# Kernel tuning notes

Measured on AMD Instinct MI355X. Metric: run time of the kernel, lower is better.

Reference implementation:

```python
import jax, jax.numpy as jnp
import numpy as np

OBS_DIM, GOAL_DIM, NUM_SKILLS, ACTION_DIM = 256, 64, 16, 32
HIDDEN = 128
BATCH = 65536


def setup_inputs() -> dict:
    key = jax.random.key(0)
    ks = jax.random.split(key, 10)
    s = lambda k, shape, fan_in: jax.random.normal(k, shape, jnp.float32) * (1.0 / np.sqrt(fan_in))
    return {
        "obs": jax.random.normal(ks[0], (BATCH, OBS_DIM), jnp.float32),
        "goals": jax.random.normal(ks[1], (BATCH, GOAL_DIM), jnp.float32),
        # gate (AlphaNet) params
        "Wa1": s(ks[2], (OBS_DIM + GOAL_DIM, HIDDEN), OBS_DIM + GOAL_DIM),
        "ba1": jnp.zeros((HIDDEN,), jnp.float32),
        "Wa2": s(ks[3], (HIDDEN, NUM_SKILLS), HIDDEN),
        "ba2": jnp.zeros((NUM_SKILLS,), jnp.float32),
        # stacked executor params: [S, in, out]
        "W1": s(ks[4], (NUM_SKILLS, OBS_DIM, HIDDEN), OBS_DIM),
        "b1": jnp.zeros((NUM_SKILLS, HIDDEN), jnp.float32),
        "W2": s(ks[5], (NUM_SKILLS, HIDDEN, ACTION_DIM), HIDDEN),
        "b2": jnp.zeros((NUM_SKILLS, ACTION_DIM), jnp.float32),
    }


def reference(obs, goals, Wa1, ba1, Wa2, ba2, W1, b1, W2, b2):
    # gate: softmax(Linear(ReLU(Linear(cat(obs, goals)))))
    concat_input = jnp.concatenate([obs, goals], axis=-1)  # [B, O+G]
    ha = jax.nn.relu(concat_input @ Wa1 + ba1)             # [B, H]
    alphas = jax.nn.softmax(ha @ Wa2 + ba2, axis=-1)       # [B, S]

    # all experts as one grouped GEMM over stacked weights
    h = jax.nn.relu(jnp.einsum("bo,soh->bsh", obs, W1) + b1[None])  # [B, S, H]
    skill_outputs = jnp.einsum("bsh,sha->bsa", h, W2) + b2[None]    # [B, S, A]

    # weighted sum over skills
    mixed_action = jnp.einsum("bsa,bs->ba", skill_outputs, alphas)  # [B, A]
    return mixed_action, alphas
```

## Files before the change

### kernel.cpp

```cpp
#include <hip/hip_runtime.h>


typedef __attribute__((ext_vector_type(8))) short    bf16x8;
typedef __attribute__((ext_vector_type(4))) float    f32x4;
typedef __attribute__((ext_vector_type(4))) _Float16 f16x4;
using half2v = decltype(__builtin_amdgcn_cvt_pkrtz(0.f, 0.f));

#define GATE_W1_OFF   0
#define GATE_W2_OFF   81920
#define GATE_BA1_OFF  86016
#define GATE_BA2_OFF  86528
#define GATE_BYTES    86592
#define S_W1_STRIDE   528
#define S_W2_OFF      67584
#define S_W2_STRIDE   272
#define S_B1_OFF      76288
#define S_B2_OFF      76800
#define S_IMG         76928
#define LDS_BYTES     163520

__device__ __forceinline__ unsigned short f2bf(float f) {
  unsigned u = __builtin_bit_cast(unsigned, f);
  return (unsigned short)((u + 0x7FFFu + ((u >> 16) & 1u)) >> 16);
}

__device__ __forceinline__ bf16x8 pack_bf8(f32x4 a, f32x4 b) {
  int4 r;
  asm("v_cvt_pk_bf16_f32 %0, %1, %2" : "=v"(r.x) : "v"(a[0]), "v"(a[1]));
  asm("v_cvt_pk_bf16_f32 %0, %1, %2" : "=v"(r.y) : "v"(a[2]), "v"(a[3]));
  asm("v_cvt_pk_bf16_f32 %0, %1, %2" : "=v"(r.z) : "v"(b[0]), "v"(b[1]));
  asm("v_cvt_pk_bf16_f32 %0, %1, %2" : "=v"(r.w) : "v"(b[2]), "v"(b[3]));
  return __builtin_bit_cast(bf16x8, r);
}

#define RELU_SCALE_PACK(dst, v, av, z)                                   \
  {                                                                      \
    half2v lo_ = __builtin_amdgcn_cvt_pkrtz((v)[0], (v)[1]);             \
    half2v hi_ = __builtin_amdgcn_cvt_pkrtz((v)[2], (v)[3]);             \
    lo_ = __builtin_elementwise_max(lo_, z) * (av);                      \
    hi_ = __builtin_elementwise_max(hi_, z) * (av);                      \
    dst[0] = (_Float16)lo_[0]; dst[1] = (_Float16)lo_[1];                \
    dst[2] = (_Float16)hi_[0]; dst[3] = (_Float16)hi_[1];                \
  }

__global__ void prep_weights(const float* __restrict__ Wa1, const float* __restrict__ Wa2,
                             const float* __restrict__ ba1, const float* __restrict__ ba2,
                             const float* __restrict__ W1,  const float* __restrict__ W2,
                             const float* __restrict__ b1,  const float* __restrict__ b2,
                             unsigned char* __restrict__ ws) {
  int i = blockIdx.x * 256 + threadIdx.x;
  if (i < 524288) {
    int s = i >> 15, r = i & 32767, h = r >> 8, o = r & 255;
    float v = W1[(s * 256 + o) * 128 + h];
    *(unsigned short*)(ws + GATE_BYTES + s * S_IMG + h * S_W1_STRIDE + 2 * o) = f2bf(v);
  } else if (i < 589824) {
    int j = i - 524288, s = j >> 12, r = j & 4095, a = r >> 7, h = r & 127;
    float v = W2[(s * 128 + h) * 32 + a];
    *(_Float16*)(ws + GATE_BYTES + s * S_IMG + S_W2_OFF + a * S_W2_STRIDE + 2 * h) =
        (_Float16)v;
  } else if (i < 630784) {
    int j = i - 589824, h = j / 320, o = j - h * 320;
    float v = Wa1[o * 128 + h];
    *(unsigned short*)(ws + GATE_W1_OFF + h * 640 +
                       ((2 * o) ^ ((h & 7) << 4))) = f2bf(v);
  } else if (i < 632832) {
    int j = i - 630784, n = j >> 7, h = j & 127;
    float v = Wa2[h * 16 + n];
    *(_Float16*)(ws + GATE_W2_OFF + n * 256 +
                 ((2 * h) ^ ((n & 7) << 3))) = (_Float16)v;
  } else if (i < 634880) {
    int j = i - 632832, s = j >> 7, h = j & 127;
    *(float*)(ws + GATE_BYTES + s * S_IMG + S_B1_OFF + 4 * h) = b1[s * 128 + h];
  } else if (i < 635392) {
    int j = i - 634880, s = j >> 5, a = j & 31;
    *(float*)(ws + GATE_BYTES + s * S_IMG + S_B2_OFF + 4 * a) = b2[s * 32 + a];
  } else if (i < 635520) {
    int j = i - 635392;
    *(float*)(ws + GATE_BA1_OFF + 4 * j) = ba1[j];
  } else if (i < 635536) {
    int j = i - 635520;
    *(float*)(ws + GATE_BA2_OFF + 4 * j) = ba2[j];
  }
}

__device__ __forceinline__ void stage_lin(const unsigned char* gsrc, unsigned char* ldst,
                                          int tid, int bytes) {
  for (int off = tid * 16; off < bytes; off += 512 * 16) {
    __builtin_amdgcn_global_load_lds(
        (const __attribute__((address_space(1))) unsigned int*)(const void*)(gsrc + off),
        (__attribute__((address_space(3))) unsigned int*)(void*)(ldst + off), 16, 0, 0);
  }
}

__global__ __launch_bounds__(512, 2)
void mop_fused(const float* __restrict__ obs, const float* __restrict__ goals,
               const unsigned char* __restrict__ ws, float* __restrict__ dout) {
  extern __shared__ unsigned char smem[];
  const int tid  = threadIdx.x;
  const int lane = tid & 63;
  const int wave = tid >> 6;
  const int l15  = lane & 15;
  const int g    = lane >> 4;
  const int swz4 = (lane & 7) << 4;
  const int swz3 = (lane & 7) << 3;
  const int rowbase = blockIdx.x * 256 + wave * 32;

  float* out_mixed = dout;
  float* out_alpha = dout + 65536 * 32;

  const int lw1 = l15 * S_W1_STRIDE + 16 * g;
  const int lw2 = S_W2_OFF + l15 * S_W2_STRIDE + 8 * g;
  const int lb  = 16 * g;

  stage_lin(ws, smem, tid, GATE_BYTES);

  bf16x8 obsf[2][8];
  bf16x8 goalf[2][2];
  #pragma unroll
  for (int nb = 0; nb < 2; ++nb) {
    const float* rp = obs + (size_t)(rowbase + nb * 16 + l15) * 256 + 8 * g;
    #pragma unroll
    for (int t = 0; t < 8; ++t) {
      f32x4 a = *(const f32x4*)(rp + 32 * t);
      f32x4 c = *(const f32x4*)(rp + 32 * t + 4);
      obsf[nb][t] = pack_bf8(a, c);
    }
    const float* gp = goals + (size_t)(rowbase + nb * 16 + l15) * 64 + 8 * g;
    #pragma unroll
    for (int t = 0; t < 2; ++t) {
      f32x4 a = *(const f32x4*)(gp + 32 * t);
      f32x4 c = *(const f32x4*)(gp + 32 * t + 4);
      goalf[nb][t] = pack_bf8(a, c);
    }
  }

  __syncthreads();

  stage_lin(ws + GATE_BYTES, smem + GATE_BYTES, tid, S_IMG);

  f32x4 gacc[2][8];
  #pragma unroll
  for (int ht = 0; ht < 8; ++ht) {
    f32x4 bias = *(const f32x4*)(smem + GATE_BA1_OFF + 64 * ht + lb);
    gacc[0][ht] = bias; gacc[1][ht] = bias;
  }
  #pragma unroll
  for (int t = 0; t < 10; ++t) {
    bf16x8 bf0 = (t < 8) ? obsf[0][t] : goalf[0][t - 8];
    bf16x8 bf1 = (t < 8) ? obsf[1][t] : goalf[1][t - 8];
    #pragma unroll
    for (int ht = 0; ht < 8; ++ht) {
      int row = 16 * ht + l15;
      bf16x8 af = *(const bf16x8*)(smem + GATE_W1_OFF + row * 640 +
                                   ((64 * t + 16 * g) ^ swz4));
      gacc[0][ht] = __builtin_amdgcn_mfma_f32_16x16x32_bf16(af, bf0, gacc[0][ht], 0, 0, 0);
      gacc[1][ht] = __builtin_amdgcn_mfma_f32_16x16x32_bf16(af, bf1, gacc[1][ht], 0, 0, 0);
    }
  }

  const half2v zh = __builtin_amdgcn_cvt_pkrtz(0.f, 0.f);
  f32x4 alph[2];
  #pragma unroll
  for (int nb = 0; nb < 2; ++nb) {
    f32x4 lacc = *(const f32x4*)(smem + GATE_BA2_OFF + lb);
    #pragma unroll
    for (int ht = 0; ht < 8; ++ht) {
      f32x4 v = gacc[nb][ht];
      f16x4 hf;
      {
        half2v lo_ = __builtin_amdgcn_cvt_pkrtz(v[0], v[1]);
        half2v hi_ = __builtin_amdgcn_cvt_pkrtz(v[2], v[3]);
        lo_ = __builtin_elementwise_max(lo_, zh);
        hi_ = __builtin_elementwise_max(hi_, zh);
        hf[0] = (_Float16)lo_[0]; hf[1] = (_Float16)lo_[1];
        hf[2] = (_Float16)hi_[0]; hf[3] = (_Float16)hi_[1];
      }
      f16x4 wf = *(const f16x4*)(smem + GATE_W2_OFF + l15 * 256 +
                                 ((32 * ht + 8 * g) ^ swz3));
      lacc = __builtin_amdgcn_mfma_f32_16x16x16f16(wf, hf, lacc, 0, 0, 0);
    }
    float m = fmaxf(fmaxf(lacc[0], lacc[1]), fmaxf(lacc[2], lacc[3]));
    m = fmaxf(m, __shfl_xor(m, 16, 64));
    m = fmaxf(m, __shfl_xor(m, 32, 64));
    f32x4 e;
    e[0] = __expf(lacc[0] - m); e[1] = __expf(lacc[1] - m);
    e[2] = __expf(lacc[2] - m); e[3] = __expf(lacc[3] - m);
    float ssum = e[0] + e[1] + e[2] + e[3];
    ssum += __shfl_xor(ssum, 16, 64);
    ssum += __shfl_xor(ssum, 32, 64);
    float inv = 1.0f / ssum;
    alph[nb] = e * inv;
    *(f32x4*)(out_alpha + (size_t)(rowbase + nb * 16 + l15) * 16 + 4 * g) = alph[nb];
  }

  __syncthreads();

  f32x4 macc[2][2] = {};
  for (int s = 0; s < 16; ++s) {
    const unsigned char* buf = smem + ((s & 1) ? 0 : GATE_BYTES);
    if (s < 15) {
      unsigned char* nbuf = smem + (((s + 1) & 1) ? 0 : GATE_BYTES);
      stage_lin(ws + GATE_BYTES + (size_t)(s + 1) * S_IMG, nbuf, tid, S_IMG);
    }
    f32x4 acc[2][8];
    #pragma unroll
    for (int ht = 0; ht < 8; ++ht) {
      f32x4 b1v = *(const f32x4*)(buf + S_B1_OFF + 64 * ht + lb);
      acc[0][ht] = b1v; acc[1][ht] = b1v;
    }

    const int asrc = ((s >> 2) << 4) | l15;
    float p0 = (s & 1) ? alph[0][1] : alph[0][0];
    float p1 = (s & 1) ? alph[0][3] : alph[0][2];
    float as0 = __shfl((s & 2) ? p1 : p0, asrc, 64);
    float q0 = (s & 1) ? alph[1][1] : alph[1][0];
    float q1 = (s & 1) ? alph[1][3] : alph[1][2];
    float as1 = __shfl((s & 2) ? q1 : q0, asrc, 64);
    const half2v a0h = __builtin_amdgcn_cvt_pkrtz(as0, as0);
    const half2v a1h = __builtin_amdgcn_cvt_pkrtz(as1, as1);

    const unsigned char* w1p = buf + lw1;
    const unsigned char* w2p = buf + lw2;

    __builtin_amdgcn_s_setprio(1);
    #pragma unroll
    for (int t = 0; t < 8; ++t) {
      const unsigned char* w1t = w1p + t * 64;
      #pragma unroll
      for (int ht = 0; ht < 8; ++ht) {
        bf16x8 af = *(const bf16x8*)(w1t + ht * 8448);
        acc[0][ht] = __builtin_amdgcn_mfma_f32_16x16x32_bf16(af, obsf[0][t], acc[0][ht], 0, 0, 0);
        acc[1][ht] = __builtin_amdgcn_mfma_f32_16x16x32_bf16(af, obsf[1][t], acc[1][ht], 0, 0, 0);
      }
    }
    #pragma unroll
    for (int ht = 0; ht < 8; ++ht) {
      f16x4 hf0, hf1;
      RELU_SCALE_PACK(hf0, acc[0][ht], a0h, zh);
      RELU_SCALE_PACK(hf1, acc[1][ht], a1h, zh);
      #pragma unroll
      for (int ta = 0; ta < 2; ++ta) {
        f16x4 wf = *(const f16x4*)(w2p + ta * 4352 + ht * 32);
        macc[0][ta] = __builtin_amdgcn_mfma_f32_16x16x16f16(wf, hf0, macc[0][ta], 0, 0, 0);
        macc[1][ta] = __builtin_amdgcn_mfma_f32_16x16x16f16(wf, hf1, macc[1][ta], 0, 0, 0);
      }
    }
    __builtin_amdgcn_s_setprio(0);
    #pragma unroll
    for (int ta = 0; ta < 2; ++ta) {
      f32x4 b2v = *(const f32x4*)(buf + S_B2_OFF + 64 * ta + lb);
      macc[0][ta] = macc[0][ta] + b2v * as0;
      macc[1][ta] = macc[1][ta] + b2v * as1;
    }
    __syncthreads();
  }

  #pragma unroll
  for (int nb = 0; nb < 2; ++nb) {
    #pragma unroll
    for (int ta = 0; ta < 2; ++ta) {
      *(f32x4*)(out_mixed + (size_t)(rowbase + nb * 16 + l15) * 32 + 16 * ta + 4 * g) =
          macc[nb][ta];
    }
  }
}

extern "C" void kernel_launch(void* const* d_in, const int* in_sizes, int n_in,
                              void* d_out, int out_size, void* d_ws, size_t ws_size,
                              hipStream_t stream) {
  const float* obs   = (const float*)d_in[0];
  const float* goals = (const float*)d_in[1];
  const float* Wa1   = (const float*)d_in[2];
  const float* ba1   = (const float*)d_in[3];
  const float* Wa2   = (const float*)d_in[4];
  const float* ba2   = (const float*)d_in[5];
  const float* W1    = (const float*)d_in[6];
  const float* b1    = (const float*)d_in[7];
  const float* W2    = (const float*)d_in[8];
  const float* b2    = (const float*)d_in[9];
  unsigned char* ws  = (unsigned char*)d_ws;
  float* out = (float*)d_out;

  prep_weights<<<2483, 256, 0, stream>>>(Wa1, Wa2, ba1, ba2, W1, W2, b1, b2, ws);
  mop_fused<<<256, 512, LDS_BYTES, stream>>>(obs, goals, ws, out);
}
```

Measured before the change: 93.70 us.

## Software-pipeline skill loop across halves and hoist biases into a single LDS block

Splits each skill's hidden dimension into two halves and defers the second half's ReLU/scale and second GEMM into the next iteration. This interleaves the W1 MFMA chain with W2 MFMAs and places the next-skill weight staging between the two halves. Biases for all skills are staged once into a separate LDS region, with b2 stored as bf16, which shrinks the per-skill image. The aim is to hide the dependency and latency of the second-layer GEMMs and the staging. The cost is an extra barrier per iteration, more live registers, and bf16 rounding of b2.

```diff
diff --git a/kernel.cpp b/kernel.cpp
--- a/kernel.cpp
+++ b/kernel.cpp
@@ -4,6 +4,7 @@
 typedef __attribute__((ext_vector_type(8))) short    bf16x8;
 typedef __attribute__((ext_vector_type(4))) float    f32x4;
 typedef __attribute__((ext_vector_type(4))) _Float16 f16x4;
+typedef __attribute__((ext_vector_type(4))) short    s16x4;
 using half2v = decltype(__builtin_amdgcn_cvt_pkrtz(0.f, 0.f));
 
 #define GATE_W1_OFF   0
@@ -14,14 +15,21 @@
 #define S_W1_STRIDE   528
 #define S_W2_OFF      67584
 #define S_W2_STRIDE   272
-#define S_B1_OFF      76288
-#define S_B2_OFF      76800
-#define S_IMG         76928
-#define LDS_BYTES     163520
+#define S_IMG         76288
+#define BIAS_LDS      76928
+#define B2_LDS        85120
+#define BIAS_BYTES    9216
+#define LDS_BYTES     162880
+#define BIAS_WS       1307200
 
 __device__ __forceinline__ unsigned short f2bf(float f) {
   unsigned u = __builtin_bit_cast(unsigned, f);
   return (unsigned short)((u + 0x7FFFu + ((u >> 16) & 1u)) >> 16);
+}
+
+__device__ __forceinline__ float bf2f(short s) {
+  unsigned u = ((unsigned)(unsigned short)s) << 16;
+  return __builtin_bit_cast(float, u);
 }
 
 __device__ __forceinline__ bf16x8 pack_bf8(f32x4 a, f32x4 b) {
@@ -69,11 +77,11 @@
     *(_Float16*)(ws + GATE_W2_OFF + n * 256 +
                  ((2 * h) ^ ((n & 7) << 3))) = (_Float16)v;
   } else if (i < 634880) {
-    int j = i - 632832, s = j >> 7, h = j & 127;
-    *(float*)(ws + GATE_BYTES + s * S_IMG + S_B1_OFF + 4 * h) = b1[s * 128 + h];
+    int j = i - 632832;
+    *(float*)(ws + BIAS_WS + 4 * j) = b1[j];
   } else if (i < 635392) {
-    int j = i - 634880, s = j >> 5, a = j & 31;
-    *(float*)(ws + GATE_BYTES + s * S_IMG + S_B2_OFF + 4 * a) = b2[s * 32 + a];
+    int j = i - 634880;
+    *(unsigned short*)(ws + BIAS_WS + 8192 + 2 * j) = f2bf(b2[j]);
   } else if (i < 635520) {
     int j = i - 635392;
     *(float*)(ws + GATE_BA1_OFF + 4 * j) = ba1[j];
@@ -195,20 +203,26 @@
 
   __syncthreads();
 
+  stage_lin(ws + BIAS_WS, smem + BIAS_LDS, tid, BIAS_BYTES);
+
+  f32x4 accA[2][4], accB[2][4];
   f32x4 macc[2][2] = {};
+  half2v a0hP = zh, a1hP = zh;
+  float as0P = 0.f, as1P = 0.f;
+  const unsigned char* w2pP = smem;
+
   for (int s = 0; s < 16; ++s) {
     const unsigned char* buf = smem + ((s & 1) ? 0 : GATE_BYTES);
-    if (s < 15) {
-      unsigned char* nbuf = smem + (((s + 1) & 1) ? 0 : GATE_BYTES);
-      stage_lin(ws + GATE_BYTES + (size_t)(s + 1) * S_IMG, nbuf, tid, S_IMG);
-    }
-    f32x4 acc[2][8];
-    #pragma unroll
-    for (int ht = 0; ht < 8; ++ht) {
-      f32x4 b1v = *(const f32x4*)(buf + S_B1_OFF + 64 * ht + lb);
-      acc[0][ht] = b1v; acc[1][ht] = b1v;
-    }
-
+    const unsigned char* w1p = buf + lw1;
+    const unsigned char* w2p = buf + lw2;
+
+    __syncthreads();
+
+    __builtin_amdgcn_s_setprio(1);
+    f32x4 b1v[8];
+    #pragma unroll
+    for (int ht = 0; ht < 8; ++ht)
+      b1v[ht] = *(const f32x4*)(smem + BIAS_LDS + s * 512 + 64 * ht + lb);
     const int asrc = ((s >> 2) << 4) | l15;
     float p0 = (s & 1) ? alph[0][1] : alph[0][0];
     float p1 = (s & 1) ? alph[0][3] : alph[0][2];
@@ -219,40 +233,100 @@
     const half2v a0h = __builtin_amdgcn_cvt_pkrtz(as0, as0);
     const half2v a1h = __builtin_amdgcn_cvt_pkrtz(as1, as1);
 
-    const unsigned char* w1p = buf + lw1;
-    const unsigned char* w2p = buf + lw2;
-
-    __builtin_amdgcn_s_setprio(1);
+    #pragma unroll
+    for (int hl = 0; hl < 4; ++hl) { accA[0][hl] = b1v[hl]; accA[1][hl] = b1v[hl]; }
     #pragma unroll
     for (int t = 0; t < 8; ++t) {
       const unsigned char* w1t = w1p + t * 64;
       #pragma unroll
-      for (int ht = 0; ht < 8; ++ht) {
-        bf16x8 af = *(const bf16x8*)(w1t + ht * 8448);
-        acc[0][ht] = __builtin_amdgcn_mfma_f32_16x16x32_bf16(af, obsf[0][t], acc[0][ht], 0, 0, 0);
-        acc[1][ht] = __builtin_amdgcn_mfma_f32_16x16x32_bf16(af, obsf[1][t], acc[1][ht], 0, 0, 0);
-      }
-    }
-    #pragma unroll
-    for (int ht = 0; ht < 8; ++ht) {
+      for (int hl = 0; hl < 4; ++hl) {
+        bf16x8 af = *(const bf16x8*)(w1t + hl * 8448);
+        accA[0][hl] = __builtin_amdgcn_mfma_f32_16x16x32_bf16(af, obsf[0][t], accA[0][hl], 0, 0, 0);
+        accA[1][hl] = __builtin_amdgcn_mfma_f32_16x16x32_bf16(af, obsf[1][t], accA[1][hl], 0, 0, 0);
+      }
+    }
+    if (s > 0) {
+      #pragma unroll
+      for (int hl = 0; hl < 4; ++hl) {
+        f16x4 hf0, hf1;
+        RELU_SCALE_PACK(hf0, accB[0][hl], a0hP, zh);
+        RELU_SCALE_PACK(hf1, accB[1][hl], a1hP, zh);
+        #pragma unroll
+        for (int ta = 0; ta < 2; ++ta) {
+          f16x4 wf = *(const f16x4*)(w2pP + ta * 4352 + (4 + hl) * 32);
+          macc[0][ta] = __builtin_amdgcn_mfma_f32_16x16x16f16(wf, hf0, macc[0][ta], 0, 0, 0);
+          macc[1][ta] = __builtin_amdgcn_mfma_f32_16x16x16f16(wf, hf1, macc[1][ta], 0, 0, 0);
+        }
+      }
+      #pragma unroll
+      for (int ta = 0; ta < 2; ++ta) {
+        s16x4 raw = *(const s16x4*)(smem + B2_LDS + (s - 1) * 64 + (16 * ta + 4 * g) * 2);
+        f32x4 b2v;
+        b2v[0] = bf2f(raw[0]); b2v[1] = bf2f(raw[1]);
+        b2v[2] = bf2f(raw[2]); b2v[3] = bf2f(raw[3]);
+        macc[0][ta] = macc[0][ta] + b2v * as0P;
+        macc[1][ta] = macc[1][ta] + b2v * as1P;
+      }
+    }
+    __builtin_amdgcn_s_setprio(0);
+
+    __syncthreads();
+
+    if (s < 15) {
+      unsigned char* nbuf = smem + (((s + 1) & 1) ? 0 : GATE_BYTES);
+      stage_lin(ws + GATE_BYTES + (size_t)(s + 1) * S_IMG, nbuf, tid, S_IMG);
+    }
+
+    __builtin_amdgcn_s_setprio(1);
+    #pragma unroll
+    for (int hl = 0; hl < 4; ++hl) { accB[0][hl] = b1v[4 + hl]; accB[1][hl] = b1v[4 + hl]; }
+    #pragma unroll
+    for (int t = 0; t < 8; ++t) {
+      const unsigned char* w1t = w1p + t * 64;
+      #pragma unroll
+      for (int hl = 0; hl < 4; ++hl) {
+        bf16x8 af = *(const bf16x8*)(w1t + (4 + hl) * 8448);
+        accB[0][hl] = __builtin_amdgcn_mfma_f32_16x16x32_bf16(af, obsf[0][t], accB[0][hl], 0, 0, 0);
+        accB[1][hl] = __builtin_amdgcn_mfma_f32_16x16x32_bf16(af, obsf[1][t], accB[1][hl], 0, 0, 0);
+      }
+    }
+    #pragma unroll
+    for (int hl = 0; hl < 4; ++hl) {
       f16x4 hf0, hf1;
-      RELU_SCALE_PACK(hf0, acc[0][ht], a0h, zh);
-      RELU_SCALE_PACK(hf1, acc[1][ht], a1h, zh);
+      RELU_SCALE_PACK(hf0, accA[0][hl], a0h, zh);
+      RELU_SCALE_PACK(hf1, accA[1][hl], a1h, zh);
       #pragma unroll
       for (int ta = 0; ta < 2; ++ta) {
-        f16x4 wf = *(const f16x4*)(w2p + ta * 4352 + ht * 32);
+        f16x4 wf = *(const f16x4*)(w2p + ta * 4352 + hl * 32);
         macc[0][ta] = __builtin_amdgcn_mfma_f32_16x16x16f16(wf, hf0, macc[0][ta], 0, 0, 0);
         macc[1][ta] = __builtin_amdgcn_mfma_f32_16x16x16f16(wf, hf1, macc[1][ta], 0, 0, 0);
       }
     }
     __builtin_amdgcn_s_setprio(0);
+
+    a0hP = a0h; a1hP = a1h; as0P = as0; as1P = as1; w2pP = w2p;
+  }
+
+  #pragma unroll
+  for (int hl = 0; hl < 4; ++hl) {
+    f16x4 hf0, hf1;
+    RELU_SCALE_PACK(hf0, accB[0][hl], a0hP, zh);
+    RELU_SCALE_PACK(hf1, accB[1][hl], a1hP, zh);
     #pragma unroll
     for (int ta = 0; ta < 2; ++ta) {
-      f32x4 b2v = *(const f32x4*)(buf + S_B2_OFF + 64 * ta + lb);
-      macc[0][ta] = macc[0][ta] + b2v * as0;
-      macc[1][ta] = macc[1][ta] + b2v * as1;
-    }
-    __syncthreads();
+      f16x4 wf = *(const f16x4*)(w2pP + ta * 4352 + (4 + hl) * 32);
+      macc[0][ta] = __builtin_amdgcn_mfma_f32_16x16x16f16(wf, hf0, macc[0][ta], 0, 0, 0);
+      macc[1][ta] = __builtin_amdgcn_mfma_f32_16x16x16f16(wf, hf1, macc[1][ta], 0, 0, 0);
+    }
+  }
+  #pragma unroll
+  for (int ta = 0; ta < 2; ++ta) {
+    s16x4 raw = *(const s16x4*)(smem + B2_LDS + 15 * 64 + (16 * ta + 4 * g) * 2);
+    f32x4 b2v;
+    b2v[0] = bf2f(raw[0]); b2v[1] = bf2f(raw[1]);
+    b2v[2] = bf2f(raw[2]); b2v[3] = bf2f(raw[3]);
+    macc[0][ta] = macc[0][ta] + b2v * as0P;
+    macc[1][ta] = macc[1][ta] + b2v * as1P;
   }
 
   #pragma unroll
```

Measured after the change: 94.62 us. Within noise of the previous version (+1.0%).

## Switch executor GEMMs to 32x32x16 MFMA with permuted weight layout

Applied to the files above, without the earlier changes.

The per-skill executor matmuls move from 16x16x32 and 16x16x16 MFMA tiles to 32x32x16 bf16/f16 MFMA. The prep kernel permutes W1 rows, b1 and b2 so the 32x32 accumulator layout feeds the second GEMM directly. Obs is reloaded from global in a 32-row fragment layout. The mixed output is transposed through an LDS scratch area so each store is a contiguous row. The aim is fewer MFMA issues and fewer weight LDS reads per FLOP, at the cost of a second global read of obs and extra LDS traffic in the epilogue.

```diff
diff --git a/kernel.cpp b/kernel.cpp
--- a/kernel.cpp
+++ b/kernel.cpp
@@ -1,9 +1,11 @@
 #include <hip/hip_runtime.h>
 
 
-typedef __attribute__((ext_vector_type(8))) short    bf16x8;
-typedef __attribute__((ext_vector_type(4))) float    f32x4;
-typedef __attribute__((ext_vector_type(4))) _Float16 f16x4;
+typedef __attribute__((ext_vector_type(8)))  short    bf16x8;
+typedef __attribute__((ext_vector_type(4)))  float    f32x4;
+typedef __attribute__((ext_vector_type(16))) float    f32x16;
+typedef __attribute__((ext_vector_type(4)))  _Float16 f16x4;
+typedef __attribute__((ext_vector_type(8)))  _Float16 f16x8;
 using half2v = decltype(__builtin_amdgcn_cvt_pkrtz(0.f, 0.f));
 
 #define GATE_W1_OFF   0
@@ -33,16 +35,6 @@
   return __builtin_bit_cast(bf16x8, r);
 }
 
-#define RELU_SCALE_PACK(dst, v, av, z)                                   \
-  {                                                                      \
-    half2v lo_ = __builtin_amdgcn_cvt_pkrtz((v)[0], (v)[1]);             \
-    half2v hi_ = __builtin_amdgcn_cvt_pkrtz((v)[2], (v)[3]);             \
-    lo_ = __builtin_elementwise_max(lo_, z) * (av);                      \
-    hi_ = __builtin_elementwise_max(hi_, z) * (av);                      \
-    dst[0] = (_Float16)lo_[0]; dst[1] = (_Float16)lo_[1];                \
-    dst[2] = (_Float16)hi_[0]; dst[3] = (_Float16)hi_[1];                \
-  }
-
 __global__ void prep_weights(const float* __restrict__ Wa1, const float* __restrict__ Wa2,
                              const float* __restrict__ ba1, const float* __restrict__ ba2,
                              const float* __restrict__ W1,  const float* __restrict__ W2,
@@ -51,8 +43,9 @@
   int i = blockIdx.x * 256 + threadIdx.x;
   if (i < 524288) {
     int s = i >> 15, r = i & 32767, h = r >> 8, o = r & 255;
+    int hp = (h & ~12) | ((h & 4) << 1) | ((h & 8) >> 1);
     float v = W1[(s * 256 + o) * 128 + h];
-    *(unsigned short*)(ws + GATE_BYTES + s * S_IMG + h * S_W1_STRIDE + 2 * o) = f2bf(v);
+    *(unsigned short*)(ws + GATE_BYTES + s * S_IMG + hp * S_W1_STRIDE + 2 * o) = f2bf(v);
   } else if (i < 589824) {
     int j = i - 524288, s = j >> 12, r = j & 4095, a = r >> 7, h = r & 127;
     float v = W2[(s * 128 + h) * 32 + a];
@@ -70,10 +63,12 @@
                  ((2 * h) ^ ((n & 7) << 3))) = (_Float16)v;
   } else if (i < 634880) {
     int j = i - 632832, s = j >> 7, h = j & 127;
-    *(float*)(ws + GATE_BYTES + s * S_IMG + S_B1_OFF + 4 * h) = b1[s * 128 + h];
+    int hp = (h & ~12) | ((h & 4) << 1) | ((h & 8) >> 1);
+    *(float*)(ws + GATE_BYTES + s * S_IMG + S_B1_OFF + 4 * hp) = b1[s * 128 + h];
   } else if (i < 635392) {
-    int j = i - 634880, s = j >> 5, a = j & 31;
-    *(float*)(ws + GATE_BYTES + s * S_IMG + S_B2_OFF + 4 * a) = b2[s * 32 + a];
+    int j = i - 634880, s = j >> 5, p = j & 31;
+    int a = (p & 3) | ((p & 4) << 1) | ((p & 8) << 1) | ((p & 16) >> 2);
+    *(float*)(ws + GATE_BYTES + s * S_IMG + S_B2_OFF + 4 * p) = b2[s * 32 + a];
   } else if (i < 635520) {
     int j = i - 635392;
     *(float*)(ws + GATE_BA1_OFF + 4 * j) = ba1[j];
@@ -101,6 +96,8 @@
   const int wave = tid >> 6;
   const int l15  = lane & 15;
   const int g    = lane >> 4;
+  const int r31  = lane & 31;
+  const int hi   = lane >> 5;
   const int swz4 = (lane & 7) << 4;
   const int swz3 = (lane & 7) << 3;
   const int rowbase = blockIdx.x * 256 + wave * 32;
@@ -108,107 +105,110 @@
   float* out_mixed = dout;
   float* out_alpha = dout + 65536 * 32;
 
-  const int lw1 = l15 * S_W1_STRIDE + 16 * g;
-  const int lw2 = S_W2_OFF + l15 * S_W2_STRIDE + 8 * g;
-  const int lb  = 16 * g;
-
   stage_lin(ws, smem, tid, GATE_BYTES);
-
-  bf16x8 obsf[2][8];
-  bf16x8 goalf[2][2];
-  #pragma unroll
-  for (int nb = 0; nb < 2; ++nb) {
-    const float* rp = obs + (size_t)(rowbase + nb * 16 + l15) * 256 + 8 * g;
-    #pragma unroll
-    for (int t = 0; t < 8; ++t) {
-      f32x4 a = *(const f32x4*)(rp + 32 * t);
-      f32x4 c = *(const f32x4*)(rp + 32 * t + 4);
-      obsf[nb][t] = pack_bf8(a, c);
-    }
-    const float* gp = goals + (size_t)(rowbase + nb * 16 + l15) * 64 + 8 * g;
-    #pragma unroll
-    for (int t = 0; t < 2; ++t) {
-      f32x4 a = *(const f32x4*)(gp + 32 * t);
-      f32x4 c = *(const f32x4*)(gp + 32 * t + 4);
-      goalf[nb][t] = pack_bf8(a, c);
-    }
-  }
-
-  __syncthreads();
-
-  stage_lin(ws + GATE_BYTES, smem + GATE_BYTES, tid, S_IMG);
-
-  f32x4 gacc[2][8];
-  #pragma unroll
-  for (int ht = 0; ht < 8; ++ht) {
-    f32x4 bias = *(const f32x4*)(smem + GATE_BA1_OFF + 64 * ht + lb);
-    gacc[0][ht] = bias; gacc[1][ht] = bias;
-  }
-  #pragma unroll
-  for (int t = 0; t < 10; ++t) {
-    bf16x8 bf0 = (t < 8) ? obsf[0][t] : goalf[0][t - 8];
-    bf16x8 bf1 = (t < 8) ? obsf[1][t] : goalf[1][t - 8];
-    #pragma unroll
-    for (int ht = 0; ht < 8; ++ht) {
-      int row = 16 * ht + l15;
-      bf16x8 af = *(const bf16x8*)(smem + GATE_W1_OFF + row * 640 +
-                                   ((64 * t + 16 * g) ^ swz4));
-      gacc[0][ht] = __builtin_amdgcn_mfma_f32_16x16x32_bf16(af, bf0, gacc[0][ht], 0, 0, 0);
-      gacc[1][ht] = __builtin_amdgcn_mfma_f32_16x16x32_bf16(af, bf1, gacc[1][ht], 0, 0, 0);
-    }
-  }
 
   const half2v zh = __builtin_amdgcn_cvt_pkrtz(0.f, 0.f);
   f32x4 alph[2];
-  #pragma unroll
-  for (int nb = 0; nb < 2; ++nb) {
-    f32x4 lacc = *(const f32x4*)(smem + GATE_BA2_OFF + lb);
+  {
+    bf16x8 gobs[2][8];
+    bf16x8 goalf[2][2];
+    #pragma unroll
+    for (int nb = 0; nb < 2; ++nb) {
+      const float* rp = obs + (size_t)(rowbase + nb * 16 + l15) * 256 + 8 * g;
+      #pragma unroll
+      for (int t = 0; t < 8; ++t) {
+        f32x4 a = *(const f32x4*)(rp + 32 * t);
+        f32x4 c = *(const f32x4*)(rp + 32 * t + 4);
+        gobs[nb][t] = pack_bf8(a, c);
+      }
+      const float* gp = goals + (size_t)(rowbase + nb * 16 + l15) * 64 + 8 * g;
+      #pragma unroll
+      for (int t = 0; t < 2; ++t) {
+        f32x4 a = *(const f32x4*)(gp + 32 * t);
+        f32x4 c = *(const f32x4*)(gp + 32 * t + 4);
+        goalf[nb][t] = pack_bf8(a, c);
+      }
+    }
+
+    __syncthreads();
+    stage_lin(ws + GATE_BYTES, smem + GATE_BYTES, tid, S_IMG);
+
+    f32x4 gacc[2][8];
     #pragma unroll
     for (int ht = 0; ht < 8; ++ht) {
-      f32x4 v = gacc[nb][ht];
-      f16x4 hf;
-      {
-        half2v lo_ = __builtin_amdgcn_cvt_pkrtz(v[0], v[1]);
-        half2v hi_ = __builtin_amdgcn_cvt_pkrtz(v[2], v[3]);
-        lo_ = __builtin_elementwise_max(lo_, zh);
-        hi_ = __builtin_elementwise_max(hi_, zh);
-        hf[0] = (_Float16)lo_[0]; hf[1] = (_Float16)lo_[1];
-        hf[2] = (_Float16)hi_[0]; hf[3] = (_Float16)hi_[1];
-      }
-      f16x4 wf = *(const f16x4*)(smem + GATE_W2_OFF + l15 * 256 +
-                                 ((32 * ht + 8 * g) ^ swz3));
-      lacc = __builtin_amdgcn_mfma_f32_16x16x16f16(wf, hf, lacc, 0, 0, 0);
-    }
-    float m = fmaxf(fmaxf(lacc[0], lacc[1]), fmaxf(lacc[2], lacc[3]));
-    m = fmaxf(m, __shfl_xor(m, 16, 64));
-    m = fmaxf(m, __shfl_xor(m, 32, 64));
-    f32x4 e;
-    e[0] = __expf(lacc[0] - m); e[1] = __expf(lacc[1] - m);
-    e[2] = __expf(lacc[2] - m); e[3] = __expf(lacc[3] - m);
-    float ssum = e[0] + e[1] + e[2] + e[3];
-    ssum += __shfl_xor(ssum, 16, 64);
-    ssum += __shfl_xor(ssum, 32, 64);
-    float inv = 1.0f / ssum;
-    alph[nb] = e * inv;
-    *(f32x4*)(out_alpha + (size_t)(rowbase + nb * 16 + l15) * 16 + 4 * g) = alph[nb];
+      f32x4 bias = *(const f32x4*)(smem + GATE_BA1_OFF + 64 * ht + 16 * g);
+      gacc[0][ht] = bias; gacc[1][ht] = bias;
+    }
+    #pragma unroll
+    for (int t = 0; t < 10; ++t) {
+      bf16x8 bf0 = (t < 8) ? gobs[0][t] : goalf[0][t - 8];
+      bf16x8 bf1 = (t < 8) ? gobs[1][t] : goalf[1][t - 8];
+      #pragma unroll
+      for (int ht = 0; ht < 8; ++ht) {
+        int row = 16 * ht + l15;
+        bf16x8 af = *(const bf16x8*)(smem + GATE_W1_OFF + row * 640 +
+                                     ((64 * t + 16 * g) ^ swz4));
+        gacc[0][ht] = __builtin_amdgcn_mfma_f32_16x16x32_bf16(af, bf0, gacc[0][ht], 0, 0, 0);
+        gacc[1][ht] = __builtin_amdgcn_mfma_f32_16x16x32_bf16(af, bf1, gacc[1][ht], 0, 0, 0);
+      }
+    }
+    #pragma unroll
+    for (int nb = 0; nb < 2; ++nb) {
+      f32x4 lacc = *(const f32x4*)(smem + GATE_BA2_OFF + 16 * g);
+      #pragma unroll
+      for (int ht = 0; ht < 8; ++ht) {
+        f32x4 v = gacc[nb][ht];
+        f16x4 hf;
+        {
+          half2v lo_ = __builtin_amdgcn_cvt_pkrtz(v[0], v[1]);
+          half2v hi_ = __builtin_amdgcn_cvt_pkrtz(v[2], v[3]);
+          lo_ = __builtin_elementwise_max(lo_, zh);
+          hi_ = __builtin_elementwise_max(hi_, zh);
+          hf[0] = (_Float16)lo_[0]; hf[1] = (_Float16)lo_[1];
+          hf[2] = (_Float16)hi_[0]; hf[3] = (_Float16)hi_[1];
+        }
+        f16x4 wf = *(const f16x4*)(smem + GATE_W2_OFF + l15 * 256 +
+                                   ((32 * ht + 8 * g) ^ swz3));
+        lacc = __builtin_amdgcn_mfma_f32_16x16x16f16(wf, hf, lacc, 0, 0, 0);
+      }
+      float m = fmaxf(fmaxf(lacc[0], lacc[1]), fmaxf(lacc[2], lacc[3]));
+      m = fmaxf(m, __shfl_xor(m, 16, 64));
+      m = fmaxf(m, __shfl_xor(m, 32, 64));
+      f32x4 e;
+      e[0] = __expf(lacc[0] - m); e[1] = __expf(lacc[1] - m);
+      e[2] = __expf(lacc[2] - m); e[3] = __expf(lacc[3] - m);
+      float ssum = e[0] + e[1] + e[2] + e[3];
+      ssum += __shfl_xor(ssum, 16, 64);
+      ssum += __shfl_xor(ssum, 32, 64);
+      float inv = 1.0f / ssum;
+      alph[nb] = e * inv;
+      *(f32x4*)(out_alpha + (size_t)(rowbase + nb * 16 + l15) * 16 + 4 * g) = alph[nb];
+    }
+  }
+
+  bf16x8 obsf[16];
+  {
+    const float* rp2 = obs + (size_t)(rowbase + r31) * 256 + 8 * hi;
+    #pragma unroll
+    for (int t = 0; t < 16; ++t) {
+      f32x4 a = *(const f32x4*)(rp2 + 16 * t);
+      f32x4 c = *(const f32x4*)(rp2 + 16 * t + 4);
+      obsf[t] = pack_bf8(a, c);
+    }
   }
 
   __syncthreads();
 
-  f32x4 macc[2][2] = {};
+  const int lw1 = r31 * S_W1_STRIDE + 16 * hi;
+  const int lw2 = S_W2_OFF + r31 * S_W2_STRIDE + 16 * hi;
+
+  f32x16 macc = {};
   for (int s = 0; s < 16; ++s) {
     const unsigned char* buf = smem + ((s & 1) ? 0 : GATE_BYTES);
     if (s < 15) {
       unsigned char* nbuf = smem + (((s + 1) & 1) ? 0 : GATE_BYTES);
       stage_lin(ws + GATE_BYTES + (size_t)(s + 1) * S_IMG, nbuf, tid, S_IMG);
     }
-    f32x4 acc[2][8];
-    #pragma unroll
-    for (int ht = 0; ht < 8; ++ht) {
-      f32x4 b1v = *(const f32x4*)(buf + S_B1_OFF + 64 * ht + lb);
-      acc[0][ht] = b1v; acc[1][ht] = b1v;
-    }
-
     const int asrc = ((s >> 2) << 4) | l15;
     float p0 = (s & 1) ? alph[0][1] : alph[0][0];
     float p1 = (s & 1) ? alph[0][3] : alph[0][2];
@@ -216,52 +216,84 @@
     float q0 = (s & 1) ? alph[1][1] : alph[1][0];
     float q1 = (s & 1) ? alph[1][3] : alph[1][2];
     float as1 = __shfl((s & 2) ? q1 : q0, asrc, 64);
-    const half2v a0h = __builtin_amdgcn_cvt_pkrtz(as0, as0);
-    const half2v a1h = __builtin_amdgcn_cvt_pkrtz(as1, as1);
+    const float av = (r31 >> 4) ? as1 : as0;
+    const half2v avh = __builtin_amdgcn_cvt_pkrtz(av, av);
 
     const unsigned char* w1p = buf + lw1;
     const unsigned char* w2p = buf + lw2;
 
+    f32x16 acc[4];
+    #pragma unroll
+    for (int ht = 0; ht < 4; ++ht) {
+      f32x4 c0 = *(const f32x4*)(buf + S_B1_OFF + (32 * ht + 4 * hi) * 4);
+      f32x4 c1 = *(const f32x4*)(buf + S_B1_OFF + (32 * ht + 8 + 4 * hi) * 4);
+      f32x4 c2 = *(const f32x4*)(buf + S_B1_OFF + (32 * ht + 16 + 4 * hi) * 4);
+      f32x4 c3 = *(const f32x4*)(buf + S_B1_OFF + (32 * ht + 24 + 4 * hi) * 4);
+      acc[ht][0]  = c0[0]; acc[ht][1]  = c0[1]; acc[ht][2]  = c0[2]; acc[ht][3]  = c0[3];
+      acc[ht][4]  = c1[0]; acc[ht][5]  = c1[1]; acc[ht][6]  = c1[2]; acc[ht][7]  = c1[3];
+      acc[ht][8]  = c2[0]; acc[ht][9]  = c2[1]; acc[ht][10] = c2[2]; acc[ht][11] = c2[3];
+      acc[ht][12] = c3[0]; acc[ht][13] = c3[1]; acc[ht][14] = c3[2]; acc[ht][15] = c3[3];
+    }
+
     __builtin_amdgcn_s_setprio(1);
     #pragma unroll
-    for (int t = 0; t < 8; ++t) {
-      const unsigned char* w1t = w1p + t * 64;
-      #pragma unroll
-      for (int ht = 0; ht < 8; ++ht) {
-        bf16x8 af = *(const bf16x8*)(w1t + ht * 8448);
-        acc[0][ht] = __builtin_amdgcn_mfma_f32_16x16x32_bf16(af, obsf[0][t], acc[0][ht], 0, 0, 0);
-        acc[1][ht] = __builtin_amdgcn_mfma_f32_16x16x32_bf16(af, obsf[1][t], acc[1][ht], 0, 0, 0);
-      }
-    }
-    #pragma unroll
-    for (int ht = 0; ht < 8; ++ht) {
-      f16x4 hf0, hf1;
-      RELU_SCALE_PACK(hf0, acc[0][ht], a0h, zh);
-      RELU_SCALE_PACK(hf1, acc[1][ht], a1h, zh);
-      #pragma unroll
-      for (int ta = 0; ta < 2; ++ta) {
-        f16x4 wf = *(const f16x4*)(w2p + ta * 4352 + ht * 32);
-        macc[0][ta] = __builtin_amdgcn_mfma_f32_16x16x16f16(wf, hf0, macc[0][ta], 0, 0, 0);
-        macc[1][ta] = __builtin_amdgcn_mfma_f32_16x16x16f16(wf, hf1, macc[1][ta], 0, 0, 0);
+    for (int t = 0; t < 16; ++t) {
+      const unsigned char* w1t = w1p + t * 32;
+      #pragma unroll
+      for (int ht = 0; ht < 4; ++ht) {
+        bf16x8 af = *(const bf16x8*)(w1t + ht * 16896);
+        acc[ht] = __builtin_amdgcn_mfma_f32_32x32x16_bf16(af, obsf[t], acc[ht], 0, 0, 0);
+      }
+    }
+    #pragma unroll
+    for (int ht = 0; ht < 4; ++ht) {
+      #pragma unroll
+      for (int q = 0; q < 2; ++q) {
+        const int t2 = 2 * ht + q;
+        int4 w;
+        {
+          half2v h0 = __builtin_amdgcn_cvt_pkrtz(acc[ht][8 * q + 0], acc[ht][8 * q + 1]);
+          half2v h1 = __builtin_amdgcn_cvt_pkrtz(acc[ht][8 * q + 2], acc[ht][8 * q + 3]);
+          half2v h2 = __builtin_amdgcn_cvt_pkrtz(acc[ht][8 * q + 4], acc[ht][8 * q + 5]);
+          half2v h3 = __builtin_amdgcn_cvt_pkrtz(acc[ht][8 * q + 6], acc[ht][8 * q + 7]);
+          h0 = __builtin_elementwise_max(h0, zh) * avh;
+          h1 = __builtin_elementwise_max(h1, zh) * avh;
+          h2 = __builtin_elementwise_max(h2, zh) * avh;
+          h3 = __builtin_elementwise_max(h3, zh) * avh;
+          w.x = __builtin_bit_cast(int, h0); w.y = __builtin_bit_cast(int, h1);
+          w.z = __builtin_bit_cast(int, h2); w.w = __builtin_bit_cast(int, h3);
+        }
+        f16x8 hf = __builtin_bit_cast(f16x8, w);
+        f16x8 w2f = *(const f16x8*)(w2p + t2 * 32);
+        macc = __builtin_amdgcn_mfma_f32_32x32x16_f16(w2f, hf, macc, 0, 0, 0);
       }
     }
     __builtin_amdgcn_s_setprio(0);
-    #pragma unroll
-    for (int ta = 0; ta < 2; ++ta) {
-      f32x4 b2v = *(const f32x4*)(buf + S_B2_OFF + 64 * ta + lb);
-      macc[0][ta] = macc[0][ta] + b2v * as0;
-      macc[1][ta] = macc[1][ta] + b2v * as1;
+    {
+      f32x4 d0 = *(const f32x4*)(buf + S_B2_OFF + (16 * hi + 0) * 4);
+      f32x4 d1 = *(const f32x4*)(buf + S_B2_OFF + (16 * hi + 4) * 4);
+      f32x4 d2 = *(const f32x4*)(buf + S_B2_OFF + (16 * hi + 8) * 4);
+      f32x4 d3 = *(const f32x4*)(buf + S_B2_OFF + (16 * hi + 12) * 4);
+      macc[0]  += av * d0[0]; macc[1]  += av * d0[1]; macc[2]  += av * d0[2]; macc[3]  += av * d0[3];
+      macc[4]  += av * d1[0]; macc[5]  += av * d1[1]; macc[6]  += av * d1[2]; macc[7]  += av * d1[3];
+      macc[8]  += av * d2[0]; macc[9]  += av * d2[1]; macc[10] += av * d2[2]; macc[11] += av * d2[3];
+      macc[12] += av * d3[0]; macc[13] += av * d3[1]; macc[14] += av * d3[2]; macc[15] += av * d3[3];
     }
     __syncthreads();
   }
 
+  unsigned char* scr = smem + wave * 4352;
   #pragma unroll
-  for (int nb = 0; nb < 2; ++nb) {
-    #pragma unroll
-    for (int ta = 0; ta < 2; ++ta) {
-      *(f32x4*)(out_mixed + (size_t)(rowbase + nb * 16 + l15) * 32 + 16 * ta + 4 * g) =
-          macc[nb][ta];
-    }
+  for (int r = 0; r < 16; ++r) {
+    const int a = (r & 3) | ((r & 4) << 1) | ((r & 8) << 1) | (hi << 2);
+    *(float*)(scr + (r31 * 33 + a) * 4) = macc[r];
+  }
+  __syncthreads();
+  const int r2 = lane >> 1, c16 = (lane & 1) * 16;
+  #pragma unroll
+  for (int k = 0; k < 4; ++k) {
+    f32x4 v = *(const f32x4*)(scr + (r2 * 33 + c16 + 4 * k) * 4);
+    *(f32x4*)(out_mixed + (size_t)(rowbase + r2) * 32 + c16 + 4 * k) = v;
   }
 }
 
```

After: 103.3 us. 10.3% more time.

## Split fused kernel into separate gate and skill-expert kernels

Applied to the files above, without the earlier changes.

The single fused kernel is split into a gate kernel that writes alphas to the output buffer and a skill kernel that reads them back from global memory. The skill kernel uses 256-thread blocks with a single-buffered LDS image of about 77KB, so two blocks can share a CU instead of one large block. The weight staging is no longer double-buffered: each expert's weights are loaded after the previous compute finishes, behind two barriers, so load latency is exposed. It also adds an extra kernel launch, reloads obs in both kernels, and does scalar global reads of alpha on every skill iteration.

```diff
diff --git a/kernel.cpp b/kernel.cpp
--- a/kernel.cpp
+++ b/kernel.cpp
@@ -17,7 +17,6 @@
 #define S_B1_OFF      76288
 #define S_B2_OFF      76800
 #define S_IMG         76928
-#define LDS_BYTES     163520
 
 __device__ __forceinline__ unsigned short f2bf(float f) {
   unsigned u = __builtin_bit_cast(unsigned, f);
@@ -83,18 +82,19 @@
   }
 }
 
+template <int NT>
 __device__ __forceinline__ void stage_lin(const unsigned char* gsrc, unsigned char* ldst,
                                           int tid, int bytes) {
-  for (int off = tid * 16; off < bytes; off += 512 * 16) {
+  for (int off = tid * 16; off < bytes; off += NT * 16) {
     __builtin_amdgcn_global_load_lds(
         (const __attribute__((address_space(1))) unsigned int*)(const void*)(gsrc + off),
         (__attribute__((address_space(3))) unsigned int*)(void*)(ldst + off), 16, 0, 0);
   }
 }
 
-__global__ __launch_bounds__(512, 2)
-void mop_fused(const float* __restrict__ obs, const float* __restrict__ goals,
-               const unsigned char* __restrict__ ws, float* __restrict__ dout) {
+__global__ __launch_bounds__(512, 1)
+void mop_gate(const float* __restrict__ obs, const float* __restrict__ goals,
+              const unsigned char* __restrict__ ws, float* __restrict__ dout) {
   extern __shared__ unsigned char smem[];
   const int tid  = threadIdx.x;
   const int lane = tid & 63;
@@ -105,14 +105,9 @@
   const int swz3 = (lane & 7) << 3;
   const int rowbase = blockIdx.x * 256 + wave * 32;
 
-  float* out_mixed = dout;
   float* out_alpha = dout + 65536 * 32;
 
-  const int lw1 = l15 * S_W1_STRIDE + 16 * g;
-  const int lw2 = S_W2_OFF + l15 * S_W2_STRIDE + 8 * g;
-  const int lb  = 16 * g;
-
-  stage_lin(ws, smem, tid, GATE_BYTES);
+  stage_lin<512>(ws, smem, tid, GATE_BYTES);
 
   bf16x8 obsf[2][8];
   bf16x8 goalf[2][2];
@@ -136,12 +131,10 @@
 
   __syncthreads();
 
-  stage_lin(ws + GATE_BYTES, smem + GATE_BYTES, tid, S_IMG);
-
   f32x4 gacc[2][8];
   #pragma unroll
   for (int ht = 0; ht < 8; ++ht) {
-    f32x4 bias = *(const f32x4*)(smem + GATE_BA1_OFF + 64 * ht + lb);
+    f32x4 bias = *(const f32x4*)(smem + GATE_BA1_OFF + 64 * ht + 16 * g);
     gacc[0][ht] = bias; gacc[1][ht] = bias;
   }
   #pragma unroll
@@ -159,10 +152,9 @@
   }
 
   const half2v zh = __builtin_amdgcn_cvt_pkrtz(0.f, 0.f);
-  f32x4 alph[2];
   #pragma unroll
   for (int nb = 0; nb < 2; ++nb) {
-    f32x4 lacc = *(const f32x4*)(smem + GATE_BA2_OFF + lb);
+    f32x4 lacc = *(const f32x4*)(smem + GATE_BA2_OFF + 16 * g);
     #pragma unroll
     for (int ht = 0; ht < 8; ++ht) {
       f32x4 v = gacc[nb][ht];
@@ -189,38 +181,62 @@
     ssum += __shfl_xor(ssum, 16, 64);
     ssum += __shfl_xor(ssum, 32, 64);
     float inv = 1.0f / ssum;
-    alph[nb] = e * inv;
-    *(f32x4*)(out_alpha + (size_t)(rowbase + nb * 16 + l15) * 16 + 4 * g) = alph[nb];
-  }
-
+    f32x4 al = e * inv;
+    *(f32x4*)(out_alpha + (size_t)(rowbase + nb * 16 + l15) * 16 + 4 * g) = al;
+  }
+}
+
+__global__ __launch_bounds__(256, 2)
+void mop_skill(const float* __restrict__ obs, const unsigned char* __restrict__ ws,
+               float* __restrict__ dout) {
+  extern __shared__ unsigned char smem[];
+  const int tid  = threadIdx.x;
+  const int lane = tid & 63;
+  const int wave = tid >> 6;
+  const int l15  = lane & 15;
+  const int g    = lane >> 4;
+  const int rowbase = blockIdx.x * 128 + wave * 32;
+
+  float* out_mixed = dout;
+  const float* alpha_in = dout + 65536 * 32;
+
+  const int lw1 = l15 * S_W1_STRIDE + 16 * g;
+  const int lw2 = S_W2_OFF + l15 * S_W2_STRIDE + 8 * g;
+  const int lb  = 16 * g;
+
+  stage_lin<256>(ws + GATE_BYTES, smem, tid, S_IMG);
+
+  bf16x8 obsf[2][8];
+  #pragma unroll
+  for (int nb = 0; nb < 2; ++nb) {
+    const float* rp = obs + (size_t)(rowbase + nb * 16 + l15) * 256 + 8 * g;
+    #pragma unroll
+    for (int t = 0; t < 8; ++t) {
+      f32x4 a = *(const f32x4*)(rp + 32 * t);
+      f32x4 c = *(const f32x4*)(rp + 32 * t + 4);
+      obsf[nb][t] = pack_bf8(a, c);
+    }
+  }
+
+  const half2v zh = __builtin_amdgcn_cvt_pkrtz(0.f, 0.f);
   __syncthreads();
 
   f32x4 macc[2][2] = {};
   for (int s = 0; s < 16; ++s) {
-    const unsigned char* buf = smem + ((s & 1) ? 0 : GATE_BYTES);
-    if (s < 15) {
-      unsigned char* nbuf = smem + (((s + 1) & 1) ? 0 : GATE_BYTES);
-      stage_lin(ws + GATE_BYTES + (size_t)(s + 1) * S_IMG, nbuf, tid, S_IMG);
-    }
-    f32x4 acc[2][8];
-    #pragma unroll
-    for (int ht = 0; ht < 8; ++ht) {
-      f32x4 b1v = *(const f32x4*)(buf + S_B1_OFF + 64 * ht + lb);
-      acc[0][ht] = b1v; acc[1][ht] = b1v;
-    }
-
-    const int asrc = ((s >> 2) << 4) | l15;
-    float p0 = (s & 1) ? alph[0][1] : alph[0][0];
-    float p1 = (s & 1) ? alph[0][3] : alph[0][2];
-    float as0 = __shfl((s & 2) ? p1 : p0, asrc, 64);
-    float q0 = (s & 1) ? alph[1][1] : alph[1][0];
-    float q1 = (s & 1) ? alph[1][3] : alph[1][2];
-    float as1 = __shfl((s & 2) ? q1 : q0, asrc, 64);
+    float as0 = alpha_in[(size_t)(rowbase + l15) * 16 + s];
+    float as1 = alpha_in[(size_t)(rowbase + 16 + l15) * 16 + s];
     const half2v a0h = __builtin_amdgcn_cvt_pkrtz(as0, as0);
     const half2v a1h = __builtin_amdgcn_cvt_pkrtz(as1, as1);
 
-    const unsigned char* w1p = buf + lw1;
-    const unsigned char* w2p = buf + lw2;
+    f32x4 acc[2][8];
+    #pragma unroll
+    for (int ht = 0; ht < 8; ++ht) {
+      f32x4 b1v = *(const f32x4*)(smem + S_B1_OFF + 64 * ht + lb);
+      acc[0][ht] = b1v; acc[1][ht] = b1v;
+    }
+
+    const unsigned char* w1p = smem + lw1;
+    const unsigned char* w2p = smem + lw2;
 
     __builtin_amdgcn_s_setprio(1);
     #pragma unroll
@@ -248,11 +264,16 @@
     __builtin_amdgcn_s_setprio(0);
     #pragma unroll
     for (int ta = 0; ta < 2; ++ta) {
-      f32x4 b2v = *(const f32x4*)(buf + S_B2_OFF + 64 * ta + lb);
+      f32x4 b2v = *(const f32x4*)(smem + S_B2_OFF + 64 * ta + lb);
       macc[0][ta] = macc[0][ta] + b2v * as0;
       macc[1][ta] = macc[1][ta] + b2v * as1;
     }
+
     __syncthreads();
+    if (s < 15) {
+      stage_lin<256>(ws + GATE_BYTES + (size_t)(s + 1) * S_IMG, smem, tid, S_IMG);
+      __syncthreads();
+    }
   }
 
   #pragma unroll
@@ -282,5 +303,6 @@
   float* out = (float*)d_out;
 
   prep_weights<<<2483, 256, 0, stream>>>(Wa1, Wa2, ba1, ba2, W1, W2, b1, b2, ws);
-  mop_fused<<<256, 512, LDS_BYTES, stream>>>(obs, goals, ws, out);
-}
+  mop_gate<<<256, 512, GATE_BYTES, stream>>>(obs, goals, ws, out);
+  mop_skill<<<512, 256, S_IMG, stream>>>(obs, ws, out);
+}
```

Measured after the change: 110.6 us. +18.1%, slower.
